# Kernel tuning notes

Hardware: AMD Instinct MI355X
Metric: run time of the kernel (lower is better)

The kernel has to match this reference:

```python
import jax, jax.numpy as jnp
import numpy as np

B, S, E = 2, 2048, 2048
H, D = 16, 128  # num_heads, head_dim = E // H


def setup_inputs() -> dict:
    key = jax.random.key(0)
    ks = jax.random.split(key, 5)
    hidden_states = jax.random.normal(ks[0], (B, S, E), dtype=jnp.float32) * 0.02
    wq = jax.random.normal(ks[1], (E, E), dtype=jnp.float32) * 0.02
    wk = jax.random.normal(ks[2], (E, E), dtype=jnp.float32) * 0.02
    wv = jax.random.normal(ks[3], (E, E), dtype=jnp.float32) * 0.02
    wo = jax.random.normal(ks[4], (E, E), dtype=jnp.float32) * 0.02
    bo = jnp.zeros((E,), dtype=jnp.float32)
    return {"hidden_states": hidden_states, "wq": wq, "wk": wk, "wv": wv, "wo": wo, "bo": bo}


def _split_heads(x):
    # [B, S, E] -> [B, H, S, D]
    return x.reshape(B, S, H, D).transpose(0, 2, 1, 3)


def reference(hidden_states, wq, wk, wv, wo, bo):
    q = _split_heads(hidden_states @ wq)  # [B,H,S,D]
    k = _split_heads(hidden_states @ wk)
    v = _split_heads(hidden_states @ wv)

    # GPT-Neo: no 1/sqrt(d) scaling; scores computed in fp32
    attn_weights = jnp.einsum("bhqd,bhkd->bhqk", q.astype(jnp.float32), k.astype(jnp.float32))

    causal_mask = jnp.tril(jnp.ones((S, S), dtype=bool))  # bias[:, :, :S, :S]
    # Faithful quirk: masked positions get the GLOBAL MIN of attn_weights, not -inf
    mask_value = jnp.min(attn_weights)
    attn_weights = jnp.where(causal_mask, attn_weights, mask_value)

    attn_weights = jax.nn.softmax(attn_weights, axis=-1).astype(v.dtype)
    attn_output = jnp.einsum("bhqk,bhkd->bhqd", attn_weights, v)  # [B,H,S,D]

    # merge heads: [B,H,S,D] -> [B,S,E]
    attn_output = attn_output.transpose(0, 2, 1, 3).reshape(B, S, E)
    attn_output = attn_output @ wo + bo
    return attn_output
```

## Files before the change

### kernel.cpp

```cpp
#include <hip/hip_runtime.h>

typedef unsigned short u16;
typedef unsigned int   u32;
typedef __attribute__((ext_vector_type(4))) float f32x4;
typedef __attribute__((ext_vector_type(4))) u32   u32x4;
typedef __attribute__((ext_vector_type(8))) __bf16 bf16x8;

#define S_LEN 2048
#define EMB   2048
#define NH    16
#define HD    128
#define NBH   32
#define MTOT  4096
#define NBMIN 512

__device__ __forceinline__ u16 f2bf(float f) {
    u32 u = __float_as_uint(f);
    return (u16)((u + 0x7FFFu + ((u >> 16) & 1u)) >> 16);
}
__device__ __forceinline__ float bf2f(u16 v) {
    return __uint_as_float(((u32)v) << 16);
}
__device__ __forceinline__ bf16x8 ld_frag(const u16* p) {
    return __builtin_bit_cast(bf16x8, *(const u32x4*)p);
}
__device__ __forceinline__ void gld_lds16(const void* g, void* l) {
    __builtin_amdgcn_global_load_lds(
        (__attribute__((address_space(1))) void*)(g),
        (__attribute__((address_space(3))) void*)(l), 16, 0, 0);
}

__global__ __launch_bounds__(256) void cast_x_kernel(
    const float* __restrict__ X, u16* __restrict__ Xb)
{
    const size_t i = ((size_t)blockIdx.x * 256 + threadIdx.x) * 8;
    float4 a = *(const float4*)&X[i];
    float4 b = *(const float4*)&X[i + 4];
    u32x4 o;
    o.x = (u32)f2bf(a.x) | ((u32)f2bf(a.y) << 16);
    o.y = (u32)f2bf(a.z) | ((u32)f2bf(a.w) << 16);
    o.z = (u32)f2bf(b.x) | ((u32)f2bf(b.y) << 16);
    o.w = (u32)f2bf(b.z) | ((u32)f2bf(b.w) << 16);
    *(u32x4*)&Xb[i] = o;
}

__global__ __launch_bounds__(256) void transpose_cast_w_kernel(
    const float* __restrict__ W0, const float* __restrict__ W1,
    const float* __restrict__ W2, const float* __restrict__ W3,
    u16* __restrict__ T0, u16* __restrict__ T1,
    u16* __restrict__ T2, u16* __restrict__ T3)
{
    __shared__ float Ls[64][68];
    const int t = threadIdx.x;
    const int n0 = blockIdx.x * 64, k0 = blockIdx.y * 64;
    const int z = blockIdx.z;
    const float* __restrict__ W = (z == 0) ? W0 : (z == 1) ? W1 : (z == 2) ? W2 : W3;
    u16* __restrict__ T = (z == 0) ? T0 : (z == 1) ? T1 : (z == 2) ? T2 : T3;

#pragma unroll
    for (int p = 0; p < 4; ++p) {
        const int r = (t >> 4) + 16 * p;
        const int c = (t & 15) * 4;
        *(float4*)&Ls[r][c] = *(const float4*)&W[(size_t)(k0 + r) * EMB + n0 + c];
    }
    __syncthreads();
    const int nl = t >> 2, q = t & 3;
    u32 pk[8];
#pragma unroll
    for (int j = 0; j < 8; ++j) {
        u16 lo = f2bf(Ls[q * 16 + 2 * j][nl]);
        u16 hi = f2bf(Ls[q * 16 + 2 * j + 1][nl]);
        pk[j] = (u32)lo | ((u32)hi << 16);
    }
    u32x4 o0 = {pk[0], pk[1], pk[2], pk[3]};
    u32x4 o1 = {pk[4], pk[5], pk[6], pk[7]};
    u16* dst = &T[(size_t)(n0 + nl) * EMB + k0 + q * 16];
    *(u32x4*)&dst[0] = o0;
    *(u32x4*)&dst[8] = o1;
}

__global__ __launch_bounds__(256) void transpose_v_kernel(
    const u16* __restrict__ V, u16* __restrict__ Vt)
{
    __shared__ u16 Ls[64][72];
    const int t = threadIdx.x;
    const int s0 = blockIdx.x * 64, d0 = blockIdx.y * 64, bh = blockIdx.z;
    const u16* __restrict__ src0 = V + ((size_t)bh * S_LEN) * HD;
    {
        const int r = t >> 2, c0 = (t & 3) * 16;
        const u16* src = &src0[(size_t)(s0 + r) * HD + d0 + c0];
        *(u32x4*)&Ls[r][c0]     = *(const u32x4*)&src[0];
        *(u32x4*)&Ls[r][c0 + 8] = *(const u32x4*)&src[8];
    }
    __syncthreads();
    const int dl = t >> 2, q = t & 3;
    u32 pk[8];
#pragma unroll
    for (int j = 0; j < 8; ++j) {
        u16 lo = Ls[q * 16 + 2 * j][dl];
        u16 hi = Ls[q * 16 + 2 * j + 1][dl];
        pk[j] = (u32)lo | ((u32)hi << 16);
    }
    u32x4 o0 = {pk[0], pk[1], pk[2], pk[3]};
    u32x4 o1 = {pk[4], pk[5], pk[6], pk[7]};
    u16* dst = &Vt[((size_t)bh * HD + d0 + dl) * S_LEN + s0 + q * 16];
    *(u32x4*)&dst[0] = o0;
    *(u32x4*)&dst[8] = o1;
}

__global__ __launch_bounds__(256) void gemm_qkv_mfma(
    const u16* __restrict__ Xb,
    const u16* __restrict__ Wtq, const u16* __restrict__ Wtk,
    const u16* __restrict__ Wtv,
    u16* __restrict__ Qo, u16* __restrict__ Ko, u16* __restrict__ Vo)
{
    __shared__ __attribute__((aligned(16))) u16 As[128 * 32];
    __shared__ __attribute__((aligned(16))) u16 Bs[128 * 32];
    const int t = threadIdx.x;
    const int w = t >> 6, lane = t & 63;
    const int wy = w >> 1, wx = w & 1;
    const int n0 = blockIdx.x * 128, m0 = blockIdx.y * 128;
    const int z = blockIdx.z;
    const u16* __restrict__ Wt = (z == 0) ? Wtq : (z == 1) ? Wtk : Wtv;
    u16* __restrict__ O = (z == 0) ? Qo : (z == 1) ? Ko : Vo;

    const int srow = lane >> 2, scol = (lane & 3) * 8;
    const u16* Ag = &Xb[(size_t)(m0 + w * 32 + srow) * EMB + scol];
    const u16* Bg = &Wt[(size_t)(n0 + w * 32 + srow) * EMB + scol];
    u16* Al0 = &As[(w * 32) * 32];
    u16* Al1 = &As[(w * 32 + 16) * 32];
    u16* Bl0 = &Bs[(w * 32) * 32];
    u16* Bl1 = &Bs[(w * 32 + 16) * 32];

    const int fm = lane & 15, fk = (lane >> 4) * 8;
    f32x4 acc[4][4];
#pragma unroll
    for (int i = 0; i < 4; ++i)
#pragma unroll
        for (int j = 0; j < 4; ++j) acc[i][j] = (f32x4)0.0f;

    for (int k0 = 0; k0 < EMB; k0 += 32) {
        __syncthreads();
        gld_lds16(Ag + k0, Al0);
        gld_lds16(Ag + 16 * EMB + k0, Al1);
        gld_lds16(Bg + k0, Bl0);
        gld_lds16(Bg + 16 * EMB + k0, Bl1);
        __syncthreads();
        bf16x8 af[4], bfr[4];
#pragma unroll
        for (int mi = 0; mi < 4; ++mi)
            af[mi] = ld_frag(&As[(64 * wy + 16 * mi + fm) * 32 + fk]);
#pragma unroll
        for (int ni = 0; ni < 4; ++ni)
            bfr[ni] = ld_frag(&Bs[(64 * wx + 16 * ni + fm) * 32 + fk]);
#pragma unroll
        for (int mi = 0; mi < 4; ++mi)
#pragma unroll
            for (int ni = 0; ni < 4; ++ni)
                acc[mi][ni] = __builtin_amdgcn_mfma_f32_16x16x32_bf16(
                    af[mi], bfr[ni], acc[mi][ni], 0, 0, 0);
    }

    const int q4 = (lane >> 4) * 4;
#pragma unroll
    for (int mi = 0; mi < 4; ++mi)
#pragma unroll
        for (int ni = 0; ni < 4; ++ni) {
            const int n = n0 + 64 * wx + 16 * ni + (lane & 15);
            const int h = n >> 7, d = n & 127;
#pragma unroll
            for (int r = 0; r < 4; ++r) {
                const int m = m0 + 64 * wy + 16 * mi + q4 + r;
                const int bb = m >> 11, s = m & 2047;
                O[(((size_t)(bb * NH + h) * S_LEN) + s) * HD + d] = f2bf(acc[mi][ni][r]);
            }
        }
}

__global__ __launch_bounds__(256) void gemm_out_mfma(
    const u16* __restrict__ Ab, const u16* __restrict__ Wto,
    const float* __restrict__ bias, float* __restrict__ Out)
{
    __shared__ __attribute__((aligned(16))) u16 As[128 * 32];
    __shared__ __attribute__((aligned(16))) u16 Bs[128 * 32];
    const int t = threadIdx.x;
    const int w = t >> 6, lane = t & 63;
    const int wy = w >> 1, wx = w & 1;
    const int n0 = blockIdx.x * 128, m0 = blockIdx.y * 128;

    const int srow = lane >> 2, scol = (lane & 3) * 8;
    const u16* Ag = &Ab[(size_t)(m0 + w * 32 + srow) * EMB + scol];
    const u16* Bg = &Wto[(size_t)(n0 + w * 32 + srow) * EMB + scol];
    u16* Al0 = &As[(w * 32) * 32];
    u16* Al1 = &As[(w * 32 + 16) * 32];
    u16* Bl0 = &Bs[(w * 32) * 32];
    u16* Bl1 = &Bs[(w * 32 + 16) * 32];

    const int fm = lane & 15, fk = (lane >> 4) * 8;
    f32x4 acc[4][4];
#pragma unroll
    for (int i = 0; i < 4; ++i)
#pragma unroll
        for (int j = 0; j < 4; ++j) acc[i][j] = (f32x4)0.0f;

    for (int k0 = 0; k0 < EMB; k0 += 32) {
        __syncthreads();
        gld_lds16(Ag + k0, Al0);
        gld_lds16(Ag + 16 * EMB + k0, Al1);
        gld_lds16(Bg + k0, Bl0);
        gld_lds16(Bg + 16 * EMB + k0, Bl1);
        __syncthreads();
        bf16x8 af[4], bfr[4];
#pragma unroll
        for (int mi = 0; mi < 4; ++mi)
            af[mi] = ld_frag(&As[(64 * wy + 16 * mi + fm) * 32 + fk]);
#pragma unroll
        for (int ni = 0; ni < 4; ++ni)
            bfr[ni] = ld_frag(&Bs[(64 * wx + 16 * ni + fm) * 32 + fk]);
#pragma unroll
        for (int mi = 0; mi < 4; ++mi)
#pragma unroll
            for (int ni = 0; ni < 4; ++ni)
                acc[mi][ni] = __builtin_amdgcn_mfma_f32_16x16x32_bf16(
                    af[mi], bfr[ni], acc[mi][ni], 0, 0, 0);
    }

    const int q4 = (lane >> 4) * 4;
#pragma unroll
    for (int mi = 0; mi < 4; ++mi)
#pragma unroll
        for (int ni = 0; ni < 4; ++ni) {
            const int n = n0 + 64 * wx + 16 * ni + (lane & 15);
            const float bv = bias[n];
#pragma unroll
            for (int r = 0; r < 4; ++r) {
                const int m = m0 + 64 * wy + 16 * mi + q4 + r;
                Out[(size_t)m * EMB + n] = acc[mi][ni][r] + bv;
            }
        }
}

__global__ __launch_bounds__(256) void reduce_min_kernel(
    const float* __restrict__ bm, float* __restrict__ minval)
{
    __shared__ float sm[256];
    const int t = threadIdx.x;
    float m = 3.0e38f;
    for (int i = t; i < NBMIN; i += 256) m = fminf(m, bm[i]);
    sm[t] = m;
    __syncthreads();
    for (int sft = 128; sft > 0; sft >>= 1) {
        if (t < sft) sm[t] = fminf(sm[t], sm[t + sft]);
        __syncthreads();
    }
    if (t == 0) minval[0] = sm[0];
}

__global__ __launch_bounds__(128) void vchunk_sum_kernel(
    const u16* __restrict__ V, float* __restrict__ csum)
{
    const int chunk = blockIdx.x, bh = blockIdx.y, d = threadIdx.x;
    const u16* vb = V + ((size_t)bh * S_LEN + chunk * 64) * HD + d;
    float s = 0.0f;
    for (int r = 0; r < 64; ++r) s += bf2f(vb[(size_t)r * HD]);
    csum[((size_t)bh * 32 + chunk) * HD + d] = s;
}

__global__ __launch_bounds__(128) void vchunk_suffix_kernel(
    const float* __restrict__ csum, float* __restrict__ csuf)
{
    const int bh = blockIdx.x, d = threadIdx.x;
    float run = 0.0f;
    for (int c = 31; c >= 0; --c) {
        const size_t idx = ((size_t)bh * 32 + c) * HD + d;
        csuf[idx] = run;
        run += csum[idx];
    }
}

__global__ __launch_bounds__(128) void vsuffix_kernel(
    const u16* __restrict__ V, const float* __restrict__ csuf,
    u16* __restrict__ vsuf)
{
    const int chunk = blockIdx.x, bh = blockIdx.y, d = threadIdx.x;
    float run = csuf[((size_t)bh * 32 + chunk) * HD + d];
    const size_t base = ((size_t)bh * S_LEN + chunk * 64) * HD + d;
    for (int r = 63; r >= 0; --r) {
        vsuf[base + (size_t)r * HD] = f2bf(run);
        run += bf2f(V[base + (size_t)r * HD]);
    }
}

__global__ __launch_bounds__(256) void attn_mfma(
    const u16* __restrict__ Q, const u16* __restrict__ K,
    const u16* __restrict__ Vt,
    u16* __restrict__ pacc0, u16* __restrict__ pacc1,
    float* __restrict__ den_p, float* __restrict__ blockmin)
{
    __shared__ __attribute__((aligned(16))) u16 Ps[128 * 136];
    __shared__ __attribute__((aligned(16))) u16 Cs[2][128 * 32];
    __shared__ float den_l[2][128];
    __shared__ float smn[256];

    const int t = threadIdx.x;
    const int w = t >> 6, lane = t & 63;
    const int wy = w >> 1, wx = w & 1;
    const int pp = blockIdx.x >> 1, hpar = blockIdx.x & 1;
    const int bh = blockIdx.y;
    const int b = bh >> 4, h = bh & 15;

    const u16* __restrict__ Kg  = K + (size_t)bh * S_LEN * HD;
    const u16* __restrict__ Vtg = Vt + (size_t)bh * HD * S_LEN;
    u16* __restrict__ pacc = hpar ? pacc1 : pacc0;

    const int srow = lane >> 2, scol = (lane & 3) * 8;
    const int fm = lane & 15, fk = (lane >> 4) * 8;
    const int q4 = (lane >> 4) * 4;

    u16* cs0a = &Cs[0][(w * 32) * 32];
    u16* cs0b = &Cs[0][(w * 32 + 16) * 32];
    u16* cs1a = &Cs[1][(w * 32) * 32];
    u16* cs1b = &Cs[1][(w * 32 + 16) * 32];

    float mn = 3.0e38f;
    int c = 0;

    {
        const u16* g = &Kg[(size_t)(hpar * 128 + w * 32 + srow) * HD + scol];
        gld_lds16(g, cs0a);
        gld_lds16(g + 16 * HD, cs0b);
    }
    __syncthreads();

    for (int pass = 0; pass < 2; ++pass) {
        const int qt = pass ? (15 - pp) : pp;
        const int i0 = qt * 128;
        const u16* __restrict__ Qg = Q + ((size_t)bh * S_LEN + i0) * HD;

        bf16x8 af[4][4];
#pragma unroll
        for (int mi = 0; mi < 4; ++mi)
#pragma unroll
            for (int dk = 0; dk < 4; ++dk)
                af[mi][dk] = ld_frag(
                    &Qg[(size_t)(64 * wy + 16 * mi + fm) * HD + dk * 32 + fk]);

        f32x4 oacc[4][4];
#pragma unroll
        for (int i = 0; i < 4; ++i)
#pragma unroll
            for (int j = 0; j < 4; ++j) oacc[i][j] = (f32x4)0.0f;
        float den[4][4] = {};

        for (int ji = 0; ji < 8; ++ji) {
            const int jt = hpar + 2 * ji;
            const int j0 = jt * 128;
            const bool causal = (jt <= qt);
            const bool last_step = (ji == 7);
            const bool have_next = (!last_step) || (pass == 0);
            const int nj0 = last_step ? hpar * 128 : (jt + 2) * 128;

            f32x4 sacc[4][4];
#pragma unroll
            for (int i = 0; i < 4; ++i)
#pragma unroll
                for (int j = 0; j < 4; ++j) sacc[i][j] = (f32x4)0.0f;

            for (int dk = 0; dk < 4; ++dk) {
                u16* na = c ? cs0a : cs1a;
                u16* nb = c ? cs0b : cs1b;
                if (dk < 3) {
                    const u16* g = &Kg[(size_t)(j0 + w * 32 + srow) * HD
                                       + (dk + 1) * 32 + scol];
                    gld_lds16(g, na);
                    gld_lds16(g + 16 * HD, nb);
                } else if (causal) {
                    const u16* g = &Vtg[(size_t)(w * 32 + srow) * S_LEN + j0 + scol];
                    gld_lds16(g, na);
                    gld_lds16(g + 16 * S_LEN, nb);
                } else if (have_next) {
                    const u16* g = &Kg[(size_t)(nj0 + w * 32 + srow) * HD + scol];
                    gld_lds16(g, na);
                    gld_lds16(g + 16 * HD, nb);
                }
                bf16x8 bfr[4];
#pragma unroll
                for (int ni = 0; ni < 4; ++ni)
                    bfr[ni] = ld_frag(&Cs[c][(64 * wx + 16 * ni + fm) * 32 + fk]);
#pragma unroll
                for (int mi = 0; mi < 4; ++mi)
#pragma unroll
                    for (int ni = 0; ni < 4; ++ni)
                        sacc[mi][ni] = __builtin_amdgcn_mfma_f32_16x16x32_bf16(
                            af[mi][dk], bfr[ni], sacc[mi][ni], 0, 0, 0);

                if (dk == 3) {
                    if (causal) {
                        const bool dg = (jt == qt);
#pragma unroll
                        for (int mi = 0; mi < 4; ++mi) {
                            const int rbase = 64 * wy + 16 * mi + q4;
#pragma unroll
                            for (int ni = 0; ni < 4; ++ni) {
                                const int cl = 64 * wx + 16 * ni + fm;
                                const int jg = j0 + cl;
#pragma unroll
                                for (int r = 0; r < 4; ++r) {
                                    const float s = sacc[mi][ni][r];
                                    mn = fminf(mn, s);
                                    float e = __expf(s);
                                    if (dg && jg > i0 + rbase + r) e = 0.0f;
                                    den[mi][r] += e;
                                    Ps[(rbase + r) * 136 + cl] = f2bf(e);
                                }
                            }
                        }
                    } else {
#pragma unroll
                        for (int mi = 0; mi < 4; ++mi)
#pragma unroll
                            for (int ni = 0; ni < 4; ++ni)
#pragma unroll
                                for (int r = 0; r < 4; ++r)
                                    mn = fminf(mn, sacc[mi][ni][r]);
                    }
                }
                __syncthreads();
                c ^= 1;
            }

            if (causal) {
                for (int sk = 0; sk < 4; ++sk) {
                    u16* na = c ? cs0a : cs1a;
                    u16* nb = c ? cs0b : cs1b;
                    if (sk < 3) {
                        const u16* g = &Vtg[(size_t)(w * 32 + srow) * S_LEN
                                            + j0 + (sk + 1) * 32 + scol];
                        gld_lds16(g, na);
                        gld_lds16(g + 16 * S_LEN, nb);
                    } else if (have_next) {
                        const u16* g = &Kg[(size_t)(nj0 + w * 32 + srow) * HD + scol];
                        gld_lds16(g, na);
                        gld_lds16(g + 16 * HD, nb);
                    }
                    bf16x8 pa[4], pb[4];
#pragma unroll
                    for (int mi = 0; mi < 4; ++mi)
                        pa[mi] = ld_frag(&Ps[(64 * wy + 16 * mi + fm) * 136
                                             + sk * 32 + fk]);
#pragma unroll
                    for (int ni = 0; ni < 4; ++ni)
                        pb[ni] = ld_frag(&Cs[c][(64 * wx + 16 * ni + fm) * 32 + fk]);
#pragma unroll
                    for (int mi = 0; mi < 4; ++mi)
#pragma unroll
                        for (int ni = 0; ni < 4; ++ni)
                            oacc[mi][ni] = __builtin_amdgcn_mfma_f32_16x16x32_bf16(
                                pa[mi], pb[ni], oacc[mi][ni], 0, 0, 0);
                    __syncthreads();
                    c ^= 1;
                }
            }
        }

#pragma unroll
        for (int mi = 0; mi < 4; ++mi)
#pragma unroll
            for (int r = 0; r < 4; ++r) {
                float v = den[mi][r];
                v += __shfl_xor(v, 1, 64);
                v += __shfl_xor(v, 2, 64);
                v += __shfl_xor(v, 4, 64);
                v += __shfl_xor(v, 8, 64);
                den[mi][r] = v;
            }
        __syncthreads();
        if ((lane & 15) == 0) {
#pragma unroll
            for (int mi = 0; mi < 4; ++mi)
#pragma unroll
                for (int r = 0; r < 4; ++r)
                    den_l[wx][64 * wy + 16 * mi + q4 + r] = den[mi][r];
        }
        __syncthreads();
        if (t < 128)
            den_p[((size_t)hpar * NBH + bh) * S_LEN + i0 + t] =
                den_l[0][t] + den_l[1][t];

#pragma unroll
        for (int mi = 0; mi < 4; ++mi)
#pragma unroll
            for (int ni = 0; ni < 4; ++ni) {
                const int d = 64 * wx + 16 * ni + fm;
#pragma unroll
                for (int r = 0; r < 4; ++r) {
                    const int row = 64 * wy + 16 * mi + q4 + r;
                    pacc[((size_t)b * S_LEN + i0 + row) * EMB + h * HD + d] =
                        f2bf(oacc[mi][ni][r]);
                }
            }
        __syncthreads();
    }

    smn[t] = mn;
    __syncthreads();
    for (int sft = 128; sft > 0; sft >>= 1) {
        if (t < sft) smn[t] = fminf(smn[t], smn[t + sft]);
        __syncthreads();
    }
    if (t == 0) blockmin[blockIdx.y * 16 + blockIdx.x] = smn[0];
}

__global__ __launch_bounds__(256) void finalize_kernel(
    u16* __restrict__ outm, const u16* __restrict__ pacc1,
    const u16* __restrict__ vsuf, const float* __restrict__ den_p,
    const float* __restrict__ minval)
{
    const size_t i = ((size_t)blockIdx.x * 256 + threadIdx.x) * 8;
    const int e = (int)(i & (EMB - 1));
    const int m = (int)(i / EMB);
    const int b = m >> 11, s = m & 2047;
    const int hh = e >> 7, d = e & 127;
    const int bh = b * NH + hh;
    const float em = __expf(minval[0]);
    const float den = den_p[(size_t)bh * S_LEN + s]
                    + den_p[((size_t)NBH + bh) * S_LEN + s]
                    + (float)(S_LEN - 1 - s) * em;
    const float inv = 1.0f / den;
    u32x4 a = *(const u32x4*)&outm[i];
    u32x4 cc = *(const u32x4*)&pacc1[i];
    u32x4 vv = *(const u32x4*)&vsuf[((size_t)bh * S_LEN + s) * HD + d];
    const u16* pa = (const u16*)&a;
    const u16* pc = (const u16*)&cc;
    const u16* pv = (const u16*)&vv;
    u16 ov[8];
#pragma unroll
    for (int j = 0; j < 8; ++j) {
        const float v = bf2f(pa[j]) + bf2f(pc[j]) + em * bf2f(pv[j]);
        ov[j] = f2bf(v * inv);
    }
    *(u32x4*)&outm[i] = *(const u32x4*)ov;
}

extern "C" void kernel_launch(void* const* d_in, const int* in_sizes, int n_in,
                              void* d_out, int out_size, void* d_ws, size_t ws_size,
                              hipStream_t stream)
{
    (void)in_sizes; (void)n_in; (void)out_size; (void)ws_size;
    const float* hs = (const float*)d_in[0];
    const float* wq = (const float*)d_in[1];
    const float* wk = (const float*)d_in[2];
    const float* wv = (const float*)d_in[3];
    const float* wo = (const float*)d_in[4];
    const float* bo = (const float*)d_in[5];
    float* out = (float*)d_out;

    char* p = (char*)d_ws;
    const size_t TS = (size_t)NBH * S_LEN * HD;
    u16* Xb   = (u16*)p; p += (size_t)MTOT * EMB * 2;
    u16* Wtq  = (u16*)p; p += (size_t)EMB * EMB * 2;
    u16* Wtk  = (u16*)p; p += (size_t)EMB * EMB * 2;
    u16* Wtv  = (u16*)p; p += (size_t)EMB * EMB * 2;
    u16* Wto  = (u16*)p; p += (size_t)EMB * EMB * 2;
    u16* Qb   = (u16*)p; p += TS * 2;
    u16* Kb   = (u16*)p; p += TS * 2;
    u16* Vb   = (u16*)p; p += TS * 2;
    u16* Vtb  = (u16*)p; p += TS * 2;
    u16* outm = (u16*)p; p += (size_t)MTOT * EMB * 2;
    u16* vsuf = (u16*)p; p += TS * 2;
    float* csum     = (float*)p; p += (size_t)NBH * 32 * HD * 4;
    float* csuf     = (float*)p; p += (size_t)NBH * 32 * HD * 4;
    float* blockmin = (float*)p; p += 1024 * 4;
    float* minval   = (float*)p; p += 64;
    float* den_p    = (float*)p; p += (size_t)2 * NBH * S_LEN * 4;
    u16* pacc1 = Xb;

    cast_x_kernel<<<4096, 256, 0, stream>>>(hs, Xb);
    transpose_cast_w_kernel<<<dim3(32, 32, 4), 256, 0, stream>>>(
        wq, wk, wv, wo, Wtq, Wtk, Wtv, Wto);

    gemm_qkv_mfma<<<dim3(EMB / 128, MTOT / 128, 3), 256, 0, stream>>>(
        Xb, Wtq, Wtk, Wtv, Qb, Kb, Vb);

    transpose_v_kernel<<<dim3(32, 2, NBH), 256, 0, stream>>>(Vb, Vtb);
    vchunk_sum_kernel<<<dim3(32, NBH), 128, 0, stream>>>(Vb, csum);
    vchunk_suffix_kernel<<<NBH, 128, 0, stream>>>(csum, csuf);
    vsuffix_kernel<<<dim3(32, NBH), 128, 0, stream>>>(Vb, csuf, vsuf);

    attn_mfma<<<dim3(16, NBH), 256, 0, stream>>>(
        Qb, Kb, Vtb, outm, pacc1, den_p, blockmin);

    reduce_min_kernel<<<1, 256, 0, stream>>>(blockmin, minval);

    finalize_kernel<<<(MTOT * EMB / 8) / 256, 256, 0, stream>>>(
        outm, pacc1, vsuf, den_p, minval);

    gemm_out_mfma<<<dim3(EMB / 128, MTOT / 128), 256, 0, stream>>>(
        outm, Wto, bo, out);
}
```

Baseline: 460.9 us.

## Triple-buffer K/V staging in attention with swizzled LDS and remapped block order

Switches the attention kernel's LDS staging from double to triple buffering with a prefetch distance of two. Each step now waits with a partial vmcnt and a raw s_barrier instead of a full __syncthreads, so global loads can overlap more MFMA work. It also XOR-swizzles the LDS column layout to cut bank conflicts and raises wave priority around the MFMA blocks. A remap of block IDs spreads heads across dispatch order, which may improve L2 locality or balance. The cost is extra LDS use, which may lower occupancy, and fragile hand-written waitcnt logic, including dummy loads on the last step.

Measured after the change: 463.2 us. About the same (+0.5%).

```diff
diff --git a/kernel.cpp b/kernel.cpp
--- a/kernel.cpp
+++ b/kernel.cpp
@@ -298,39 +298,55 @@
     float* __restrict__ den_p, float* __restrict__ blockmin)
 {
     __shared__ __attribute__((aligned(16))) u16 Ps[128 * 136];
-    __shared__ __attribute__((aligned(16))) u16 Cs[2][128 * 32];
+    __shared__ __attribute__((aligned(16))) u16 Cs[3 * 128 * 32];
     __shared__ float den_l[2][128];
     __shared__ float smn[256];
 
     const int t = threadIdx.x;
     const int w = t >> 6, lane = t & 63;
     const int wy = w >> 1, wx = w & 1;
-    const int pp = blockIdx.x >> 1, hpar = blockIdx.x & 1;
-    const int bh = blockIdx.y;
+
+    const int d_id = blockIdx.y * 16 + blockIdx.x;
+    const int f_log = (d_id & 7) * 64 + (d_id >> 3);
+    const int pp = (f_log & 15) >> 1, hpar = f_log & 1;
+    const int bh = f_log >> 4;
     const int b = bh >> 4, h = bh & 15;
 
     const u16* __restrict__ Kg  = K + (size_t)bh * S_LEN * HD;
     const u16* __restrict__ Vtg = Vt + (size_t)bh * HD * S_LEN;
     u16* __restrict__ pacc = hpar ? pacc1 : pacc0;
 
-    const int srow = lane >> 2, scol = (lane & 3) * 8;
+    const int srow = lane >> 2;
+    const int scol = ((lane & 3) ^ ((lane >> 3) & 3)) * 8;
     const int fm = lane & 15, fk = (lane >> 4) * 8;
+    const int fkc = ((lane >> 4) ^ ((fm >> 1) & 3)) * 8;
     const int q4 = (lane >> 4) * 4;
-
-    u16* cs0a = &Cs[0][(w * 32) * 32];
-    u16* cs0b = &Cs[0][(w * 32 + 16) * 32];
-    u16* cs1a = &Cs[1][(w * 32) * 32];
-    u16* cs1b = &Cs[1][(w * 32 + 16) * 32];
+    const int wrow = w * 32;
+    u16* const cs_w = Cs + wrow * 32;
+
+#define CSB(c_) (cs_w + (c_) * 4096)
+#define STAGE_K(c_, j0_, dd_) do { \
+        const u16* g_ = &Kg[(size_t)((j0_) + wrow + srow) * HD + (dd_) * 32 + scol]; \
+        gld_lds16(g_, CSB(c_)); \
+        gld_lds16(g_ + 16 * HD, CSB(c_) + 512); } while (0)
+#define STAGE_V(c_, j0_, ss_) do { \
+        const u16* g_ = &Vtg[(size_t)(wrow + srow) * S_LEN + (j0_) + (ss_) * 32 + scol]; \
+        gld_lds16(g_, CSB(c_)); \
+        gld_lds16(g_ + 16 * S_LEN, CSB(c_) + 512); } while (0)
+#define WAITBAR2() do { \
+        asm volatile("s_waitcnt lgkmcnt(0)" ::: "memory"); \
+        asm volatile("s_waitcnt vmcnt(2)" ::: "memory"); \
+        __builtin_amdgcn_s_barrier(); \
+        __builtin_amdgcn_sched_barrier(0); } while (0)
 
     float mn = 3.0e38f;
-    int c = 0;
-
-    {
-        const u16* g = &Kg[(size_t)(hpar * 128 + w * 32 + srow) * HD + scol];
-        gld_lds16(g, cs0a);
-        gld_lds16(g + 16 * HD, cs0b);
-    }
-    __syncthreads();
+    int cur = 0;
+
+    STAGE_K(0, hpar * 128, 0);
+    STAGE_K(1, hpar * 128, 1);
+    asm volatile("s_waitcnt vmcnt(2)" ::: "memory");
+    __builtin_amdgcn_s_barrier();
+    __builtin_amdgcn_sched_barrier(0);
 
     for (int pass = 0; pass < 2; ++pass) {
         const int qt = pass ? (15 - pp) : pp;
@@ -356,9 +372,8 @@
             const int jt = hpar + 2 * ji;
             const int j0 = jt * 128;
             const bool causal = (jt <= qt);
-            const bool last_step = (ji == 7);
-            const bool have_next = (!last_step) || (pass == 0);
-            const int nj0 = last_step ? hpar * 128 : (jt + 2) * 128;
+            const bool hn = (ji < 7) || (pass == 0);
+            const int nj0 = (ji < 7) ? (jt + 2) * 128 : hpar * 128;
 
             f32x4 sacc[4][4];
 #pragma unroll
@@ -366,33 +381,33 @@
 #pragma unroll
                 for (int j = 0; j < 4; ++j) sacc[i][j] = (f32x4)0.0f;
 
+#pragma unroll
             for (int dk = 0; dk < 4; ++dk) {
-                u16* na = c ? cs0a : cs1a;
-                u16* nb = c ? cs0b : cs1b;
-                if (dk < 3) {
-                    const u16* g = &Kg[(size_t)(j0 + w * 32 + srow) * HD
-                                       + (dk + 1) * 32 + scol];
-                    gld_lds16(g, na);
-                    gld_lds16(g + 16 * HD, nb);
-                } else if (causal) {
-                    const u16* g = &Vtg[(size_t)(w * 32 + srow) * S_LEN + j0 + scol];
-                    gld_lds16(g, na);
-                    gld_lds16(g + 16 * S_LEN, nb);
-                } else if (have_next) {
-                    const u16* g = &Kg[(size_t)(nj0 + w * 32 + srow) * HD + scol];
-                    gld_lds16(g, na);
-                    gld_lds16(g + 16 * HD, nb);
+                int c2 = cur - 1; if (c2 < 0) c2 += 3;
+                if (dk == 0)      STAGE_K(c2, j0, 2);
+                else if (dk == 1) STAGE_K(c2, j0, 3);
+                else if (dk == 2) {
+                    if (causal)  STAGE_V(c2, j0, 0);
+                    else if (hn) STAGE_K(c2, nj0, 0);
+                    else         STAGE_K(c2, 0, 0);
+                } else {
+                    if (causal)  STAGE_V(c2, j0, 1);
+                    else if (hn) STAGE_K(c2, nj0, 1);
+                    else         STAGE_K(c2, 0, 0);
                 }
                 bf16x8 bfr[4];
 #pragma unroll
                 for (int ni = 0; ni < 4; ++ni)
-                    bfr[ni] = ld_frag(&Cs[c][(64 * wx + 16 * ni + fm) * 32 + fk]);
+                    bfr[ni] = ld_frag(Cs + cur * 4096
+                                      + (64 * wx + 16 * ni + fm) * 32 + fkc);
+                __builtin_amdgcn_s_setprio(1);
 #pragma unroll
                 for (int mi = 0; mi < 4; ++mi)
 #pragma unroll
                     for (int ni = 0; ni < 4; ++ni)
                         sacc[mi][ni] = __builtin_amdgcn_mfma_f32_16x16x32_bf16(
                             af[mi][dk], bfr[ni], sacc[mi][ni], 0, 0, 0);
+                __builtin_amdgcn_s_setprio(0);
 
                 if (dk == 3) {
                     if (causal) {
@@ -425,23 +440,20 @@
                                     mn = fminf(mn, sacc[mi][ni][r]);
                     }
                 }
-                __syncthreads();
-                c ^= 1;
+                WAITBAR2();
+                cur = (cur == 2) ? 0 : cur + 1;
             }
 
             if (causal) {
+#pragma unroll
                 for (int sk = 0; sk < 4; ++sk) {
-                    u16* na = c ? cs0a : cs1a;
-                    u16* nb = c ? cs0b : cs1b;
-                    if (sk < 3) {
-                        const u16* g = &Vtg[(size_t)(w * 32 + srow) * S_LEN
-                                            + j0 + (sk + 1) * 32 + scol];
-                        gld_lds16(g, na);
-                        gld_lds16(g + 16 * S_LEN, nb);
-                    } else if (have_next) {
-                        const u16* g = &Kg[(size_t)(nj0 + w * 32 + srow) * HD + scol];
-                        gld_lds16(g, na);
-                        gld_lds16(g + 16 * HD, nb);
+                    int c2 = cur - 1; if (c2 < 0) c2 += 3;
+                    if (sk == 0)      STAGE_V(c2, j0, 2);
+                    else if (sk == 1) STAGE_V(c2, j0, 3);
+                    else if (sk == 2) {
+                        if (hn) STAGE_K(c2, nj0, 0); else STAGE_K(c2, 0, 0);
+                    } else {
+                        if (hn) STAGE_K(c2, nj0, 1); else STAGE_K(c2, 0, 0);
                     }
                     bf16x8 pa[4], pb[4];
 #pragma unroll
@@ -450,15 +462,18 @@
                                              + sk * 32 + fk]);
 #pragma unroll
                     for (int ni = 0; ni < 4; ++ni)
-                        pb[ni] = ld_frag(&Cs[c][(64 * wx + 16 * ni + fm) * 32 + fk]);
+                        pb[ni] = ld_frag(Cs + cur * 4096
+                                         + (64 * wx + 16 * ni + fm) * 32 + fkc);
+                    __builtin_amdgcn_s_setprio(1);
 #pragma unroll
                     for (int mi = 0; mi < 4; ++mi)
 #pragma unroll
                         for (int ni = 0; ni < 4; ++ni)
                             oacc[mi][ni] = __builtin_amdgcn_mfma_f32_16x16x32_bf16(
                                 pa[mi], pb[ni], oacc[mi][ni], 0, 0, 0);
-                    __syncthreads();
-                    c ^= 1;
+                    __builtin_amdgcn_s_setprio(0);
+                    WAITBAR2();
+                    cur = (cur == 2) ? 0 : cur + 1;
                 }
             }
         }
@@ -508,7 +523,12 @@
         if (t < sft) smn[t] = fminf(smn[t], smn[t + sft]);
         __syncthreads();
     }
-    if (t == 0) blockmin[blockIdx.y * 16 + blockIdx.x] = smn[0];
+    if (t == 0) blockmin[d_id] = smn[0];
+
+#undef CSB
+#undef STAGE_K
+#undef STAGE_V
+#undef WAITBAR2
 }
 
 __global__ __launch_bounds__(256) void finalize_kernel(
```
